# Kernel optimization log

Hardware: AMD Instinct MI355X
Metric: run time of the kernel (lower is better)

The kernel has to match this reference:

```python
import jax, jax.numpy as jnp
import numpy as np

EPS = 1e-6

def _rmsnorm(x, w):
    # RMSNorm in float32 as in the torch module, then rescale by weight
    xf = x.astype(jnp.float32)
    y = xf * jax.lax.rsqrt(jnp.mean(xf * xf, axis=-1, keepdims=True) + EPS)
    return y.astype(x.dtype) * w

def setup_inputs() -> dict:
    key = jax.random.key(0)
    k0, k1, k2 = jax.random.split(key, 3)
    B, T, C = 2, 1024, 256
    x = jax.random.normal(k0, (B, T, C), jnp.float32)
    w_qkv = jax.random.normal(k1, (3 * C, C), jnp.float32) / np.float32(np.sqrt(C))
    w_proj = jax.random.normal(k2, (C, C), jnp.float32) / np.float32(np.sqrt(C))
    qn_w = jnp.ones((2,), jnp.float32)
    kn_w = jnp.ones((2,), jnp.float32)
    return {"x": x, "w_qkv": w_qkv, "w_proj": w_proj, "qn_w": qn_w, "kn_w": kn_w}

def reference(x, w_qkv, w_proj, qn_w, kn_w):
    B, T, C = x.shape
    HD = 2                      # head_dim forced to 2 by GPTConfig invariant
    H = C // HD                 # n_head = n_embd // 2
    qkv = x @ w_qkv.T           # (B, T, 3C); Linear has bias=False
    q, k, v = jnp.split(qkv, 3, axis=-1)
    heads = lambda t: t.reshape(B, T, H, HD).transpose(0, 2, 1, 3)  # (B,H,T,2)
    q = _rmsnorm(heads(q), qn_w)
    k = _rmsnorm(heads(k), kn_w)
    v = heads(v)
    scale = np.float32(1.0 / np.sqrt(HD))
    att = jnp.einsum('bhtd,bhsd->bhts', q, k) * scale   # (B,H,T,T)
    causal = jnp.tril(jnp.ones((T, T), bool))
    att = jnp.where(causal, att, jnp.float32(-1e30))
    att = jax.nn.softmax(att, axis=-1)
    y = jnp.einsum('bhts,bhsd->bhtd', att, v)           # (B,H,T,2)
    y = y.transpose(0, 2, 1, 3).reshape(B, T, C)
    return y @ w_proj.T
```

## Files before the change

kernel.cpp:

```cpp
#include <hip/hip_runtime.h>

#define T_SEQ   1024
#define C_DIM   256
#define H_HEADS 128
#define NTOK    2048
#define BH      256

typedef unsigned short u16;
typedef unsigned int   u32;
typedef __attribute__((ext_vector_type(8))) short bf16x8;
typedef __attribute__((ext_vector_type(4))) float f32x4;
typedef __attribute__((ext_vector_type(2))) float f32x2;

typedef __attribute__((address_space(1))) u32 gu32;
typedef __attribute__((address_space(3))) u32 lu32;

__device__ __forceinline__ float bf2f(u16 u) {
  return __uint_as_float(((u32)u) << 16);
}
__device__ __forceinline__ u16 f2bf(float f) {
  u32 u = __float_as_uint(f);
  u32 r = u + 0x7fffu + ((u >> 16) & 1u);
  return (u16)(r >> 16);
}


__device__ __forceinline__ void gl_seg(const u16* g, u16* l, int lane) {
  __builtin_amdgcn_global_load_lds((gu32*)(g + lane * 8), (lu32*)l, 16, 0, 0);
}

__device__ __forceinline__ bf16x8 ldsf(const u16* plane, int row, int kk) {
  int off = (row * 128 + kk * 2) ^ ((row & 7) << 4);
  return *(const bf16x8*)((const char*)plane + off);
}

__global__ __launch_bounds__(256) void k_pack(
    const float* __restrict__ x, const float* __restrict__ wq,
    const float* __restrict__ wp,
    u16* __restrict__ xh, u16* __restrict__ xl,
    u16* __restrict__ wqh, u16* __restrict__ wql,
    u16* __restrict__ wph, u16* __restrict__ wpl)
{
  const int bid = blockIdx.x, tid = threadIdx.x;
  const float* src; u16 *dh, *dl; int ti;
  if (bid < 128)      { src = x;  dh = xh;  dl = xl;  ti = bid; }
  else if (bid < 176) { src = wq; dh = wqh; dl = wql; ti = bid - 128; }
  else                { src = wp; dh = wph; dl = wpl; ti = bid - 176; }
  const int tr = ti >> 2, kc = ti & 3;
  char* bh = (char*)dh + (size_t)ti * 8192;
  char* bl = (char*)dl + (size_t)ti * 8192;
#pragma unroll
  for (int it = 0; it < 4; ++it) {
    int idx = it * 256 + tid;
    int r = idx >> 4, c4 = (idx & 15) * 4;
    float4 g = *(const float4*)&src[(tr * 64 + r) * C_DIM + kc * 64 + c4];
    ushort4 h4, l4;
    h4.x = f2bf(g.x); l4.x = f2bf(g.x - bf2f(h4.x));
    h4.y = f2bf(g.y); l4.y = f2bf(g.y - bf2f(h4.y));
    h4.z = f2bf(g.z); l4.z = f2bf(g.z - bf2f(h4.z));
    h4.w = f2bf(g.w); l4.w = f2bf(g.w - bf2f(h4.w));
    int off = (r * 128 + c4 * 2) ^ ((r & 7) << 4);
    *(ushort4*)(bh + off) = h4;
    *(ushort4*)(bl + off) = l4;
  }
}

__global__ __launch_bounds__(256) void k_qkv(
    const u16* __restrict__ xh, const u16* __restrict__ xl,
    const u16* __restrict__ wh, const u16* __restrict__ wl,
    const float* __restrict__ qnw, const float* __restrict__ knw,
    float* __restrict__ q, float* __restrict__ kv)
{
  __shared__ __align__(16) u16 lds[2][12288];

  const int tid  = threadIdx.x;
  const int lane = tid & 63;
  const int w    = tid >> 6;
  const int bx   = blockIdx.x, by = blockIdx.y;
  const int row0 = bx * 32, col0 = by * 64;
  const int xtb  = (bx >> 1) * 4;
  const int xho  = (bx & 1) * 2048;
  const int wtb  = by * 4;
  const int fr   = lane & 15;
  const int ko   = (lane >> 4) * 8;

  f32x4 acc[2] = {};

  auto STAGE = [&](int kc, int b) {
    const u16* gxh = xh + (xtb + kc) * 4096 + xho;
    const u16* gxl = xl + (xtb + kc) * 4096 + xho;
    const u16* gwh = wh + (wtb + kc) * 4096;
    const u16* gwl = wl + (wtb + kc) * 4096;
    u16* L = lds[b];
    gl_seg(gxh + w * 512,        L + w * 512,               lane);
    gl_seg(gxl + w * 512,        L + 2048 + w * 512,        lane);
    gl_seg(gwh + w * 512,        L + 4096 + w * 512,        lane);
    gl_seg(gwh + (w + 4) * 512,  L + 4096 + (w + 4) * 512,  lane);
    gl_seg(gwl + w * 512,        L + 8192 + w * 512,        lane);
    gl_seg(gwl + (w + 4) * 512,  L + 8192 + (w + 4) * 512,  lane);
  };

  STAGE(0, 0);
  __syncthreads();
  for (int kc = 0; kc < 4; ++kc) {
    if (kc < 3) STAGE(kc + 1, (kc + 1) & 1);
    const u16* L   = lds[kc & 1];
    const u16* bXh = L;
    const u16* bXl = L + 2048;
    const u16* bWh = L + 4096;
    const u16* bWl = L + 8192;
#pragma unroll
    for (int ks = 0; ks < 2; ++ks) {
      const int kk = ks * 32 + ko;
      bf16x8 bhi = ldsf(bWh, w * 16 + fr, kk);
      bf16x8 blo = ldsf(bWl, w * 16 + fr, kk);
#pragma unroll
      for (int rt = 0; rt < 2; ++rt) {
        bf16x8 ahi = ldsf(bXh, rt * 16 + fr, kk);
        bf16x8 alo = ldsf(bXl, rt * 16 + fr, kk);
        acc[rt] = __builtin_amdgcn_mfma_f32_16x16x32_bf16(alo, bhi, acc[rt], 0, 0, 0);
        acc[rt] = __builtin_amdgcn_mfma_f32_16x16x32_bf16(ahi, blo, acc[rt], 0, 0, 0);
        acc[rt] = __builtin_amdgcn_mfma_f32_16x16x32_bf16(ahi, bhi, acc[rt], 0, 0, 0);
      }
    }
    __syncthreads();
  }

  const int sec = col0 >> 8;
  const int cg  = col0 + w * 16 + fr;
  const int d   = cg & 1;
  const int h   = (cg & 255) >> 1;
  const float wn = (sec == 0) ? qnw[d] : (sec == 1) ? knw[d] : 1.f;

#pragma unroll
  for (int rt = 0; rt < 2; ++rt) {
#pragma unroll
    for (int i = 0; i < 4; ++i) {
      float val = acc[rt][i];
      int n = row0 + rt * 16 + (lane >> 4) * 4 + i;
      int b = n >> 10, t = n & 1023;
      int bh = b * H_HEADS + h;
      if (sec < 2) {
        float pv = __shfl_xor(val, 1);
        float rr = rsqrtf(0.5f * (val * val + pv * pv) + 1e-6f);
        val = val * rr * wn;
      }
      if (sec == 0)      q [(bh * T_SEQ + t) * 2 + d]     = val;
      else if (sec == 1) kv[(bh * T_SEQ + t) * 4 + d]     = val;
      else               kv[(bh * T_SEQ + t) * 4 + 2 + d] = val;
    }
  }
}

__global__ __launch_bounds__(256) void k_attn(
    const float* __restrict__ q, const float* __restrict__ kv,
    u16* __restrict__ yh, u16* __restrict__ yl)
{
  __shared__ float4 skv[T_SEQ];
  __shared__ float  red[4][256][3];

  const int tid  = threadIdx.x;
  const int head = blockIdx.x;
  const int g    = 3 - blockIdx.y;
  const int qb   = g * 256;
  const int S    = qb + 256;
  const int lane = tid & 63;
  const int w    = tid >> 6;

  const float4* kvh = (const float4*)(kv + head * (T_SEQ * 4));
  for (int i = tid; i < S; i += 256) skv[i] = kvh[i];

  const float LS = 0.70710678118f * 1.44269504089f;
  float qxs[4], qys[4];
#pragma unroll
  for (int j = 0; j < 4; ++j) {
    int t = qb + j * 64 + lane;
    float2 qv = *(const float2*)&q[(head * T_SEQ + t) * 2];
    qxs[j] = qv.x * LS;
    qys[j] = qv.y * LS;
  }
  f32x2 qx01 = {qxs[0], qxs[1]}, qx23 = {qxs[2], qxs[3]};
  f32x2 qy01 = {qys[0], qys[1]}, qy23 = {qys[2], qys[3]};
  __syncthreads();

  f32x2 den01 = {0.f, 0.f}, den23 = {0.f, 0.f};
  f32x2 nx01  = {0.f, 0.f}, nx23  = {0.f, 0.f};
  f32x2 ny01  = {0.f, 0.f}, ny23  = {0.f, 0.f};

  const int cb = qb >> 2;
  const int b0 = w * cb, b1 = b0 + cb;
#pragma unroll 2
  for (int s = b0; s < b1; ++s) {
    float4 kvv = skv[s];
    f32x2 kx = {kvv.x, kvv.x}, ky = {kvv.y, kvv.y};
    f32x2 kz = {kvv.z, kvv.z}, kw = {kvv.w, kvv.w};
    f32x2 s01 = __builtin_elementwise_fma(qx01, kx, qy01 * ky);
    f32x2 s23 = __builtin_elementwise_fma(qx23, kx, qy23 * ky);
    f32x2 e01 = { __builtin_amdgcn_exp2f(s01.x), __builtin_amdgcn_exp2f(s01.y) };
    f32x2 e23 = { __builtin_amdgcn_exp2f(s23.x), __builtin_amdgcn_exp2f(s23.y) };
    den01 += e01; den23 += e23;
    nx01 = __builtin_elementwise_fma(e01, kz, nx01);
    nx23 = __builtin_elementwise_fma(e23, kz, nx23);
    ny01 = __builtin_elementwise_fma(e01, kw, ny01);
    ny23 = __builtin_elementwise_fma(e23, kw, ny23);
  }
  const int d0  = qb + w * 64;
  const int tqL = qb + lane;
#pragma unroll 2
  for (int s = d0; s < d0 + 64; ++s) {
    float4 kvv = skv[s];
    f32x2 kx = {kvv.x, kvv.x}, ky = {kvv.y, kvv.y};
    f32x2 kz = {kvv.z, kvv.z}, kw = {kvv.w, kvv.w};
    f32x2 s01 = __builtin_elementwise_fma(qx01, kx, qy01 * ky);
    f32x2 s23 = __builtin_elementwise_fma(qx23, kx, qy23 * ky);
    f32x2 e01 = { __builtin_amdgcn_exp2f(s01.x), __builtin_amdgcn_exp2f(s01.y) };
    f32x2 e23 = { __builtin_amdgcn_exp2f(s23.x), __builtin_amdgcn_exp2f(s23.y) };
    e01.x = (s <= tqL)       ? e01.x : 0.f;
    e01.y = (s <= tqL + 64)  ? e01.y : 0.f;
    e23.x = (s <= tqL + 128) ? e23.x : 0.f;
    e23.y = (s <= tqL + 192) ? e23.y : 0.f;
    den01 += e01; den23 += e23;
    nx01 = __builtin_elementwise_fma(e01, kz, nx01);
    nx23 = __builtin_elementwise_fma(e23, kz, nx23);
    ny01 = __builtin_elementwise_fma(e01, kw, ny01);
    ny23 = __builtin_elementwise_fma(e23, kw, ny23);
  }

  red[w][lane][0]       = den01.x; red[w][lane][1]       = nx01.x; red[w][lane][2]       = ny01.x;
  red[w][64 + lane][0]  = den01.y; red[w][64 + lane][1]  = nx01.y; red[w][64 + lane][2]  = ny01.y;
  red[w][128 + lane][0] = den23.x; red[w][128 + lane][1] = nx23.x; red[w][128 + lane][2] = ny23.x;
  red[w][192 + lane][0] = den23.y; red[w][192 + lane][1] = nx23.y; red[w][192 + lane][2] = ny23.y;
  __syncthreads();

  float dd = 0.f, ax = 0.f, ay = 0.f;
#pragma unroll
  for (int ww = 0; ww < 4; ++ww) {
    dd += red[ww][tid][0];
    ax += red[ww][tid][1];
    ay += red[ww][tid][2];
  }
  float inv = 1.f / dd;
  float ox = ax * inv, oy = ay * inv;
  int b = head >> 7, hh = head & 127;
  int t = qb + tid;
  int n = b * T_SEQ + t;
  int c = hh * 2;
  int tile = (n >> 6) * 4 + (c >> 6);
  int r = n & 63, cc = c & 63;
  int off = (r * 128 + cc * 2) ^ ((r & 7) << 4);
  u16 hx = f2bf(ox); float rx = ox - bf2f(hx);
  u16 hy = f2bf(oy); float ry = oy - bf2f(hy);
  *(u32*)((char*)yh + (size_t)tile * 8192 + off) = (u32)hx | ((u32)hy << 16);
  *(u32*)((char*)yl + (size_t)tile * 8192 + off) = (u32)f2bf(rx) | ((u32)f2bf(ry) << 16);
}

__global__ __launch_bounds__(256) void k_proj(
    const u16* __restrict__ yh, const u16* __restrict__ yl,
    const u16* __restrict__ wh, const u16* __restrict__ wl,
    float* __restrict__ out)
{
  __shared__ __align__(16) u16 lds[2][8192];

  const int tid  = threadIdx.x;
  const int lane = tid & 63;
  const int w    = tid >> 6;
  const int bx   = blockIdx.x, by = blockIdx.y;
  const int row0 = bx * 32, col0 = by * 32;
  const int ytb  = (bx >> 1) * 4;
  const int yho  = (bx & 1) * 2048;
  const int wtb  = (by >> 1) * 4;
  const int who  = (by & 1) * 2048;
  const int fr   = lane & 15;
  const int ko   = (lane >> 4) * 8;

  f32x4 acc = {};

  auto STAGE = [&](int kc, int b) {
    u16* L = lds[b];
    gl_seg(yh + (ytb + kc) * 4096 + yho + w * 512, L + w * 512,        lane);
    gl_seg(yl + (ytb + kc) * 4096 + yho + w * 512, L + 2048 + w * 512, lane);
    gl_seg(wh + (wtb + kc) * 4096 + who + w * 512, L + 4096 + w * 512, lane);
    gl_seg(wl + (wtb + kc) * 4096 + who + w * 512, L + 6144 + w * 512, lane);
  };

  STAGE(0, 0);
  __syncthreads();
  const int ar = (w >> 1) * 16 + fr;
  const int br = (w & 1) * 16 + fr;
  for (int kc = 0; kc < 4; ++kc) {
    if (kc < 3) STAGE(kc + 1, (kc + 1) & 1);
    const u16* L = lds[kc & 1];
#pragma unroll
    for (int ks = 0; ks < 2; ++ks) {
      const int kk = ks * 32 + ko;
      bf16x8 bhi = ldsf(L + 4096, br, kk);
      bf16x8 blo = ldsf(L + 6144, br, kk);
      bf16x8 ahi = ldsf(L,        ar, kk);
      bf16x8 alo = ldsf(L + 2048, ar, kk);
      acc = __builtin_amdgcn_mfma_f32_16x16x32_bf16(alo, bhi, acc, 0, 0, 0);
      acc = __builtin_amdgcn_mfma_f32_16x16x32_bf16(ahi, blo, acc, 0, 0, 0);
      acc = __builtin_amdgcn_mfma_f32_16x16x32_bf16(ahi, bhi, acc, 0, 0, 0);
    }
    __syncthreads();
  }

  const int cg = col0 + (w & 1) * 16 + fr;
#pragma unroll
  for (int i = 0; i < 4; ++i) {
    int n = row0 + (w >> 1) * 16 + (lane >> 4) * 4 + i;
    out[n * C_DIM + cg] = acc[i];
  }
}

extern "C" void kernel_launch(void* const* d_in, const int* in_sizes, int n_in,
                              void* d_out, int out_size, void* d_ws, size_t ws_size,
                              hipStream_t stream) {
  const float* x     = (const float*)d_in[0];
  const float* wqkv  = (const float*)d_in[1];
  const float* wproj = (const float*)d_in[2];
  const float* qnw   = (const float*)d_in[3];
  const float* knw   = (const float*)d_in[4];

  char* p = (char*)d_ws;
  float* q  = (float*)p;  p += (size_t)BH * T_SEQ * 2 * 4;
  float* kv = (float*)p;  p += (size_t)BH * T_SEQ * 4 * 4;
  u16* xh  = (u16*)p;     p += (size_t)NTOK  * C_DIM * 2;
  u16* xl  = (u16*)p;     p += (size_t)NTOK  * C_DIM * 2;
  u16* wqh = (u16*)p;     p += (size_t)768   * C_DIM * 2;
  u16* wql = (u16*)p;     p += (size_t)768   * C_DIM * 2;
  u16* wph = (u16*)p;     p += (size_t)C_DIM * C_DIM * 2;
  u16* wpl = (u16*)p;     p += (size_t)C_DIM * C_DIM * 2;
  u16* yh  = (u16*)p;     p += (size_t)NTOK  * C_DIM * 2;
  u16* yl  = (u16*)p;     p += (size_t)NTOK  * C_DIM * 2;

  k_pack<<<192, 256, 0, stream>>>(x, wqkv, wproj, xh, xl, wqh, wql, wph, wpl);
  k_qkv <<<dim3(64, 12), 256, 0, stream>>>(xh, xl, wqh, wql, qnw, knw, q, kv);
  k_attn<<<dim3(BH, 4),  256, 0, stream>>>(q, kv, yh, yl);
  k_proj<<<dim3(64, 8),  256, 0, stream>>>(yh, yl, wph, wpl, (float*)d_out);
}
```

Baseline: 111.6 us.

## Fuse four kernels into one persistent kernel with global atomic barriers

```diff
diff --git a/kernel.cpp b/kernel.cpp
--- a/kernel.cpp
+++ b/kernel.cpp
@@ -5,6 +5,7 @@
 #define H_HEADS 128
 #define NTOK    2048
 #define BH      256
+#define NBLK    768
 
 typedef unsigned short u16;
 typedef unsigned int   u32;
@@ -34,138 +35,30 @@
   return *(const bf16x8*)((const char*)plane + off);
 }
 
-__global__ __launch_bounds__(256) void k_pack(
-    const float* __restrict__ x, const float* __restrict__ wq,
-    const float* __restrict__ wp,
-    u16* __restrict__ xh, u16* __restrict__ xl,
-    u16* __restrict__ wqh, u16* __restrict__ wql,
-    u16* __restrict__ wph, u16* __restrict__ wpl)
+__device__ __forceinline__ void gbar(int* p, int nb) {
+  __syncthreads();
+  if (threadIdx.x == 0) {
+    __hip_atomic_fetch_add(p, 1, __ATOMIC_RELEASE, __HIP_MEMORY_SCOPE_AGENT);
+    int guard = 0;
+    while (__hip_atomic_load(p, __ATOMIC_ACQUIRE, __HIP_MEMORY_SCOPE_AGENT) < nb) {
+      __builtin_amdgcn_s_sleep(8);
+      if (++guard > (1 << 22)) break;
+    }
+    __builtin_amdgcn_fence(__ATOMIC_ACQUIRE, "agent");
+  }
+  __syncthreads();
+}
+
+__device__ __forceinline__ void attn_unit(
+    char* smem, const float* __restrict__ q, const float* __restrict__ kv,
+    u16* __restrict__ yh, u16* __restrict__ yl,
+    int head, int g, int tid, int lane, int w)
 {
-  const int bid = blockIdx.x, tid = threadIdx.x;
-  const float* src; u16 *dh, *dl; int ti;
-  if (bid < 128)      { src = x;  dh = xh;  dl = xl;  ti = bid; }
-  else if (bid < 176) { src = wq; dh = wqh; dl = wql; ti = bid - 128; }
-  else                { src = wp; dh = wph; dl = wpl; ti = bid - 176; }
-  const int tr = ti >> 2, kc = ti & 3;
-  char* bh = (char*)dh + (size_t)ti * 8192;
-  char* bl = (char*)dl + (size_t)ti * 8192;
-#pragma unroll
-  for (int it = 0; it < 4; ++it) {
-    int idx = it * 256 + tid;
-    int r = idx >> 4, c4 = (idx & 15) * 4;
-    float4 g = *(const float4*)&src[(tr * 64 + r) * C_DIM + kc * 64 + c4];
-    ushort4 h4, l4;
-    h4.x = f2bf(g.x); l4.x = f2bf(g.x - bf2f(h4.x));
-    h4.y = f2bf(g.y); l4.y = f2bf(g.y - bf2f(h4.y));
-    h4.z = f2bf(g.z); l4.z = f2bf(g.z - bf2f(h4.z));
-    h4.w = f2bf(g.w); l4.w = f2bf(g.w - bf2f(h4.w));
-    int off = (r * 128 + c4 * 2) ^ ((r & 7) << 4);
-    *(ushort4*)(bh + off) = h4;
-    *(ushort4*)(bl + off) = l4;
-  }
-}
-
-__global__ __launch_bounds__(256) void k_qkv(
-    const u16* __restrict__ xh, const u16* __restrict__ xl,
-    const u16* __restrict__ wh, const u16* __restrict__ wl,
-    const float* __restrict__ qnw, const float* __restrict__ knw,
-    float* __restrict__ q, float* __restrict__ kv)
-{
-  __shared__ __align__(16) u16 lds[2][12288];
-
-  const int tid  = threadIdx.x;
-  const int lane = tid & 63;
-  const int w    = tid >> 6;
-  const int bx   = blockIdx.x, by = blockIdx.y;
-  const int row0 = bx * 32, col0 = by * 64;
-  const int xtb  = (bx >> 1) * 4;
-  const int xho  = (bx & 1) * 2048;
-  const int wtb  = by * 4;
-  const int fr   = lane & 15;
-  const int ko   = (lane >> 4) * 8;
-
-  f32x4 acc[2] = {};
-
-  auto STAGE = [&](int kc, int b) {
-    const u16* gxh = xh + (xtb + kc) * 4096 + xho;
-    const u16* gxl = xl + (xtb + kc) * 4096 + xho;
-    const u16* gwh = wh + (wtb + kc) * 4096;
-    const u16* gwl = wl + (wtb + kc) * 4096;
-    u16* L = lds[b];
-    gl_seg(gxh + w * 512,        L + w * 512,               lane);
-    gl_seg(gxl + w * 512,        L + 2048 + w * 512,        lane);
-    gl_seg(gwh + w * 512,        L + 4096 + w * 512,        lane);
-    gl_seg(gwh + (w + 4) * 512,  L + 4096 + (w + 4) * 512,  lane);
-    gl_seg(gwl + w * 512,        L + 8192 + w * 512,        lane);
-    gl_seg(gwl + (w + 4) * 512,  L + 8192 + (w + 4) * 512,  lane);
-  };
-
-  STAGE(0, 0);
-  __syncthreads();
-  for (int kc = 0; kc < 4; ++kc) {
-    if (kc < 3) STAGE(kc + 1, (kc + 1) & 1);
-    const u16* L   = lds[kc & 1];
-    const u16* bXh = L;
-    const u16* bXl = L + 2048;
-    const u16* bWh = L + 4096;
-    const u16* bWl = L + 8192;
-#pragma unroll
-    for (int ks = 0; ks < 2; ++ks) {
-      const int kk = ks * 32 + ko;
-      bf16x8 bhi = ldsf(bWh, w * 16 + fr, kk);
-      bf16x8 blo = ldsf(bWl, w * 16 + fr, kk);
-#pragma unroll
-      for (int rt = 0; rt < 2; ++rt) {
-        bf16x8 ahi = ldsf(bXh, rt * 16 + fr, kk);
-        bf16x8 alo = ldsf(bXl, rt * 16 + fr, kk);
-        acc[rt] = __builtin_amdgcn_mfma_f32_16x16x32_bf16(alo, bhi, acc[rt], 0, 0, 0);
-        acc[rt] = __builtin_amdgcn_mfma_f32_16x16x32_bf16(ahi, blo, acc[rt], 0, 0, 0);
-        acc[rt] = __builtin_amdgcn_mfma_f32_16x16x32_bf16(ahi, bhi, acc[rt], 0, 0, 0);
-      }
-    }
-    __syncthreads();
-  }
-
-  const int sec = col0 >> 8;
-  const int cg  = col0 + w * 16 + fr;
-  const int d   = cg & 1;
-  const int h   = (cg & 255) >> 1;
-  const float wn = (sec == 0) ? qnw[d] : (sec == 1) ? knw[d] : 1.f;
-
-#pragma unroll
-  for (int rt = 0; rt < 2; ++rt) {
-#pragma unroll
-    for (int i = 0; i < 4; ++i) {
-      float val = acc[rt][i];
-      int n = row0 + rt * 16 + (lane >> 4) * 4 + i;
-      int b = n >> 10, t = n & 1023;
-      int bh = b * H_HEADS + h;
-      if (sec < 2) {
-        float pv = __shfl_xor(val, 1);
-        float rr = rsqrtf(0.5f * (val * val + pv * pv) + 1e-6f);
-        val = val * rr * wn;
-      }
-      if (sec == 0)      q [(bh * T_SEQ + t) * 2 + d]     = val;
-      else if (sec == 1) kv[(bh * T_SEQ + t) * 4 + d]     = val;
-      else               kv[(bh * T_SEQ + t) * 4 + 2 + d] = val;
-    }
-  }
-}
-
-__global__ __launch_bounds__(256) void k_attn(
-    const float* __restrict__ q, const float* __restrict__ kv,
-    u16* __restrict__ yh, u16* __restrict__ yl)
-{
-  __shared__ float4 skv[T_SEQ];
-  __shared__ float  red[4][256][3];
-
-  const int tid  = threadIdx.x;
-  const int head = blockIdx.x;
-  const int g    = 3 - blockIdx.y;
-  const int qb   = g * 256;
-  const int S    = qb + 256;
-  const int lane = tid & 63;
-  const int w    = tid >> 6;
+  float4* skv = (float4*)smem;
+  float (*red)[256][3] = (float (*)[256][3])(smem + 16384);
+
+  const int qb = g * 256;
+  const int S  = qb + 256;
 
   const float4* kvh = (const float4*)(kv + head * (T_SEQ * 4));
   for (int i = tid; i < S; i += 256) skv[i] = kvh[i];
@@ -241,9 +134,9 @@
   }
   float inv = 1.f / dd;
   float ox = ax * inv, oy = ay * inv;
-  int b = head >> 7, hh = head & 127;
+  int bb = head >> 7, hh = head & 127;
   int t = qb + tid;
-  int n = b * T_SEQ + t;
+  int n = bb * T_SEQ + t;
   int c = hh * 2;
   int tile = (n >> 6) * 4 + (c >> 6);
   int r = n & 63, cc = c & 63;
@@ -254,61 +147,185 @@
   *(u32*)((char*)yl + (size_t)tile * 8192 + off) = (u32)f2bf(rx) | ((u32)f2bf(ry) << 16);
 }
 
-__global__ __launch_bounds__(256) void k_proj(
-    const u16* __restrict__ yh, const u16* __restrict__ yl,
-    const u16* __restrict__ wh, const u16* __restrict__ wl,
-    float* __restrict__ out)
+__global__ __launch_bounds__(256, 3) void k_fused(
+    const float* __restrict__ x, const float* __restrict__ wqkv,
+    const float* __restrict__ wproj,
+    const float* __restrict__ qnw, const float* __restrict__ knw,
+    float* __restrict__ out, int* __restrict__ bar,
+    u16* __restrict__ xh, u16* __restrict__ xl,
+    u16* __restrict__ wqh, u16* __restrict__ wql,
+    u16* __restrict__ wph, u16* __restrict__ wpl,
+    float* __restrict__ q, float* __restrict__ kv,
+    u16* __restrict__ yh, u16* __restrict__ yl)
 {
-  __shared__ __align__(16) u16 lds[2][8192];
+  __shared__ __align__(16) char smem[49152];
 
   const int tid  = threadIdx.x;
+  const int blk  = blockIdx.x;
   const int lane = tid & 63;
   const int w    = tid >> 6;
-  const int bx   = blockIdx.x, by = blockIdx.y;
-  const int row0 = bx * 32, col0 = by * 32;
-  const int ytb  = (bx >> 1) * 4;
-  const int yho  = (bx & 1) * 2048;
-  const int wtb  = (by >> 1) * 4;
-  const int who  = (by & 1) * 2048;
-  const int fr   = lane & 15;
-  const int ko   = (lane >> 4) * 8;
-
-  f32x4 acc = {};
-
-  auto STAGE = [&](int kc, int b) {
-    u16* L = lds[b];
-    gl_seg(yh + (ytb + kc) * 4096 + yho + w * 512, L + w * 512,        lane);
-    gl_seg(yl + (ytb + kc) * 4096 + yho + w * 512, L + 2048 + w * 512, lane);
-    gl_seg(wh + (wtb + kc) * 4096 + who + w * 512, L + 4096 + w * 512, lane);
-    gl_seg(wl + (wtb + kc) * 4096 + who + w * 512, L + 6144 + w * 512, lane);
-  };
-
-  STAGE(0, 0);
-  __syncthreads();
-  const int ar = (w >> 1) * 16 + fr;
-  const int br = (w & 1) * 16 + fr;
-  for (int kc = 0; kc < 4; ++kc) {
-    if (kc < 3) STAGE(kc + 1, (kc + 1) & 1);
-    const u16* L = lds[kc & 1];
-#pragma unroll
-    for (int ks = 0; ks < 2; ++ks) {
-      const int kk = ks * 32 + ko;
-      bf16x8 bhi = ldsf(L + 4096, br, kk);
-      bf16x8 blo = ldsf(L + 6144, br, kk);
-      bf16x8 ahi = ldsf(L,        ar, kk);
-      bf16x8 alo = ldsf(L + 2048, ar, kk);
-      acc = __builtin_amdgcn_mfma_f32_16x16x32_bf16(alo, bhi, acc, 0, 0, 0);
-      acc = __builtin_amdgcn_mfma_f32_16x16x32_bf16(ahi, blo, acc, 0, 0, 0);
-      acc = __builtin_amdgcn_mfma_f32_16x16x32_bf16(ahi, bhi, acc, 0, 0, 0);
-    }
+
+  {
+    int ti = blk >> 2;
+    int qr = blk & 3;
+    const float* src; u16 *dh, *dl; int tt;
+    if (ti < 128)      { src = x;     dh = xh;  dl = xl;  tt = ti; }
+    else if (ti < 176) { src = wqkv;  dh = wqh; dl = wql; tt = ti - 128; }
+    else               { src = wproj; dh = wph; dl = wpl; tt = ti - 176; }
+    int tr = tt >> 2, kc = tt & 3;
+    char* bh = (char*)dh + (size_t)tt * 8192;
+    char* bl = (char*)dl + (size_t)tt * 8192;
+    int r = qr * 16 + (tid >> 4), c4 = (tid & 15) * 4;
+    float4 gv = *(const float4*)&src[(tr * 64 + r) * C_DIM + kc * 64 + c4];
+    ushort4 h4, l4;
+    h4.x = f2bf(gv.x); l4.x = f2bf(gv.x - bf2f(h4.x));
+    h4.y = f2bf(gv.y); l4.y = f2bf(gv.y - bf2f(h4.y));
+    h4.z = f2bf(gv.z); l4.z = f2bf(gv.z - bf2f(h4.z));
+    h4.w = f2bf(gv.w); l4.w = f2bf(gv.w - bf2f(h4.w));
+    int off = (r * 128 + c4 * 2) ^ ((r & 7) << 4);
+    *(ushort4*)(bh + off) = h4;
+    *(ushort4*)(bl + off) = l4;
+  }
+  gbar(bar + 0, NBLK);
+
+  {
+    u16 (*lds)[12288] = (u16 (*)[12288])smem;
+    const int bx   = blk & 63, by = blk >> 6;
+    const int row0 = bx * 32, col0 = by * 64;
+    const int xtb  = (bx >> 1) * 4;
+    const int xho  = (bx & 1) * 2048;
+    const int wtb  = by * 4;
+    const int fr   = lane & 15;
+    const int ko   = (lane >> 4) * 8;
+
+    f32x4 acc[2] = {};
+
+    auto STAGE = [&](int kc, int b) {
+      const u16* gxh = xh + (xtb + kc) * 4096 + xho;
+      const u16* gxl = xl + (xtb + kc) * 4096 + xho;
+      const u16* gwh = wqh + (wtb + kc) * 4096;
+      const u16* gwl = wql + (wtb + kc) * 4096;
+      u16* L = lds[b];
+      gl_seg(gxh + w * 512,        L + w * 512,               lane);
+      gl_seg(gxl + w * 512,        L + 2048 + w * 512,        lane);
+      gl_seg(gwh + w * 512,        L + 4096 + w * 512,        lane);
+      gl_seg(gwh + (w + 4) * 512,  L + 4096 + (w + 4) * 512,  lane);
+      gl_seg(gwl + w * 512,        L + 8192 + w * 512,        lane);
+      gl_seg(gwl + (w + 4) * 512,  L + 8192 + (w + 4) * 512,  lane);
+    };
+
+    STAGE(0, 0);
     __syncthreads();
-  }
-
-  const int cg = col0 + (w & 1) * 16 + fr;
-#pragma unroll
-  for (int i = 0; i < 4; ++i) {
-    int n = row0 + (w >> 1) * 16 + (lane >> 4) * 4 + i;
-    out[n * C_DIM + cg] = acc[i];
+    for (int kc = 0; kc < 4; ++kc) {
+      if (kc < 3) STAGE(kc + 1, (kc + 1) & 1);
+      const u16* L   = lds[kc & 1];
+      const u16* bXh = L;
+      const u16* bXl = L + 2048;
+      const u16* bWh = L + 4096;
+      const u16* bWl = L + 8192;
+#pragma unroll
+      for (int ks = 0; ks < 2; ++ks) {
+        const int kk = ks * 32 + ko;
+        bf16x8 bhi = ldsf(bWh, w * 16 + fr, kk);
+        bf16x8 blo = ldsf(bWl, w * 16 + fr, kk);
+#pragma unroll
+        for (int rt = 0; rt < 2; ++rt) {
+          bf16x8 ahi = ldsf(bXh, rt * 16 + fr, kk);
+          bf16x8 alo = ldsf(bXl, rt * 16 + fr, kk);
+          acc[rt] = __builtin_amdgcn_mfma_f32_16x16x32_bf16(alo, bhi, acc[rt], 0, 0, 0);
+          acc[rt] = __builtin_amdgcn_mfma_f32_16x16x32_bf16(ahi, blo, acc[rt], 0, 0, 0);
+          acc[rt] = __builtin_amdgcn_mfma_f32_16x16x32_bf16(ahi, bhi, acc[rt], 0, 0, 0);
+        }
+      }
+      __syncthreads();
+    }
+
+    const int sec = col0 >> 8;
+    const int cg  = col0 + w * 16 + fr;
+    const int d   = cg & 1;
+    const int h   = (cg & 255) >> 1;
+    const float wn = (sec == 0) ? qnw[d] : (sec == 1) ? knw[d] : 1.f;
+
+#pragma unroll
+    for (int rt = 0; rt < 2; ++rt) {
+#pragma unroll
+      for (int i = 0; i < 4; ++i) {
+        float val = acc[rt][i];
+        int n = row0 + rt * 16 + (lane >> 4) * 4 + i;
+        int bb = n >> 10, t = n & 1023;
+        int bh = bb * H_HEADS + h;
+        if (sec < 2) {
+          float pv = __shfl_xor(val, 1);
+          float rr = rsqrtf(0.5f * (val * val + pv * pv) + 1e-6f);
+          val = val * rr * wn;
+        }
+        if (sec == 0)      q [(bh * T_SEQ + t) * 2 + d]     = val;
+        else if (sec == 1) kv[(bh * T_SEQ + t) * 4 + d]     = val;
+        else               kv[(bh * T_SEQ + t) * 4 + 2 + d] = val;
+      }
+    }
+  }
+  gbar(bar + 1, NBLK);
+
+  {
+    const int head = blk & 255;
+    const int g1st = (blk < 256) ? 3 : (blk < 512) ? 2 : 1;
+    attn_unit(smem, q, kv, yh, yl, head, g1st, tid, lane, w);
+    if (blk >= 256 && blk < 512) {
+      __syncthreads();
+      attn_unit(smem, q, kv, yh, yl, head, 0, tid, lane, w);
+    }
+  }
+  gbar(bar + 2, NBLK);
+
+  if (blk < 512) {
+    u16 (*lds)[8192] = (u16 (*)[8192])smem;
+    const int bx   = blk & 63, by = blk >> 6;
+    const int row0 = bx * 32, col0 = by * 32;
+    const int ytb  = (bx >> 1) * 4;
+    const int yho  = (bx & 1) * 2048;
+    const int wtb  = (by >> 1) * 4;
+    const int who  = (by & 1) * 2048;
+    const int fr   = lane & 15;
+    const int ko   = (lane >> 4) * 8;
+
+    f32x4 acc = {};
+
+    auto STAGE = [&](int kc, int b) {
+      u16* L = lds[b];
+      gl_seg(yh  + (ytb + kc) * 4096 + yho + w * 512, L + w * 512,        lane);
+      gl_seg(yl  + (ytb + kc) * 4096 + yho + w * 512, L + 2048 + w * 512, lane);
+      gl_seg(wph + (wtb + kc) * 4096 + who + w * 512, L + 4096 + w * 512, lane);
+      gl_seg(wpl + (wtb + kc) * 4096 + who + w * 512, L + 6144 + w * 512, lane);
+    };
+
+    STAGE(0, 0);
+    __syncthreads();
+    const int ar = (w >> 1) * 16 + fr;
+    const int br = (w & 1) * 16 + fr;
+    for (int kc = 0; kc < 4; ++kc) {
+      if (kc < 3) STAGE(kc + 1, (kc + 1) & 1);
+      const u16* L = lds[kc & 1];
+#pragma unroll
+      for (int ks = 0; ks < 2; ++ks) {
+        const int kk = ks * 32 + ko;
+        bf16x8 bhi = ldsf(L + 4096, br, kk);
+        bf16x8 blo = ldsf(L + 6144, br, kk);
+        bf16x8 ahi = ldsf(L,        ar, kk);
+        bf16x8 alo = ldsf(L + 2048, ar, kk);
+        acc = __builtin_amdgcn_mfma_f32_16x16x32_bf16(alo, bhi, acc, 0, 0, 0);
+        acc = __builtin_amdgcn_mfma_f32_16x16x32_bf16(ahi, blo, acc, 0, 0, 0);
+        acc = __builtin_amdgcn_mfma_f32_16x16x32_bf16(ahi, bhi, acc, 0, 0, 0);
+      }
+      __syncthreads();
+    }
+
+    const int cg = col0 + (w & 1) * 16 + fr;
+#pragma unroll
+    for (int i = 0; i < 4; ++i) {
+      int n = row0 + (w >> 1) * 16 + (lane >> 4) * 4 + i;
+      out[n * C_DIM + cg] = acc[i];
+    }
   }
 }
 
@@ -322,6 +339,7 @@
   const float* knw   = (const float*)d_in[4];
 
   char* p = (char*)d_ws;
+  int* bar = (int*)p;     p += 256;
   float* q  = (float*)p;  p += (size_t)BH * T_SEQ * 2 * 4;
   float* kv = (float*)p;  p += (size_t)BH * T_SEQ * 4 * 4;
   u16* xh  = (u16*)p;     p += (size_t)NTOK  * C_DIM * 2;
@@ -333,8 +351,8 @@
   u16* yh  = (u16*)p;     p += (size_t)NTOK  * C_DIM * 2;
   u16* yl  = (u16*)p;     p += (size_t)NTOK  * C_DIM * 2;
 
-  k_pack<<<192, 256, 0, stream>>>(x, wqkv, wproj, xh, xl, wqh, wql, wph, wpl);
-  k_qkv <<<dim3(64, 12), 256, 0, stream>>>(xh, xl, wqh, wql, qnw, knw, q, kv);
-  k_attn<<<dim3(BH, 4),  256, 0, stream>>>(q, kv, yh, yl);
-  k_proj<<<dim3(64, 8),  256, 0, stream>>>(yh, yl, wph, wpl, (float*)d_out);
-}
+  (void)hipMemsetAsync(d_ws, 0, 256, stream);
+  k_fused<<<NBLK, 256, 0, stream>>>(x, wqkv, wproj, qnw, knw, (float*)d_out,
+                                    bar, xh, xl, wqh, wql, wph, wpl,
+                                    q, kv, yh, yl);
+}
```

Result: slower. 374.7 us (+235.7%).
